# Kernel optimization log

Hardware: AMD Instinct MI355X
Metric: run time of the kernel (lower is better)

The kernel has to match this reference:

```python
import jax, jax.numpy as jnp
import numpy as np

B, SM, SI, D, H, FF = 4, 1024, 4096, 256, 8, 1024
EPS = 1e-6

def _ln(x, g, b):
    m = jnp.mean(x, axis=-1, keepdims=True)
    v = jnp.mean(jnp.square(x - m), axis=-1, keepdims=True)
    return (x - m) * jax.lax.rsqrt(v + EPS) * g + b

def setup_inputs() -> dict:
    key = jax.random.key(0)
    ks = jax.random.split(key, 12)
    s = 0.02
    return {
        "state_seq": jax.random.normal(ks[0], (B, SM, D), jnp.float32),
        "input_seq": jax.random.normal(ks[1], (B, SI, D), jnp.float32),
        "Wk": jax.random.normal(ks[2], (D, D), jnp.float32) * s,
        "bk": jnp.zeros((D,), jnp.float32),
        "Wv": jax.random.normal(ks[3], (D, D), jnp.float32) * s,
        "bv": jnp.zeros((D,), jnp.float32),
        "Wq": jax.random.normal(ks[4], (H, D, D), jnp.float32) * s,
        "bq": jnp.zeros((H, D), jnp.float32),
        "Wo": jax.random.normal(ks[5], (H * D, D), jnp.float32) * s,
        "bo": jnp.zeros((D,), jnp.float32),
        "ln1_g": jnp.ones((D,), jnp.float32),
        "ln1_b": jnp.zeros((D,), jnp.float32),
        "W_in": jax.random.normal(ks[6], (D, FF), jnp.float32) * s,
        "b_in": jnp.zeros((FF,), jnp.float32),
        "Wg_nl": jax.random.normal(ks[7], (FF, FF), jnp.float32) * s,
        "bg_nl": jnp.zeros((FF,), jnp.float32),
        "Wg_l": jax.random.normal(ks[8], (FF, FF), jnp.float32) * s,
        "bg_l": jnp.zeros((FF,), jnp.float32),
        "Wg_o": jax.random.normal(ks[9], (FF, D), jnp.float32) * s,
        "bg_o": jnp.zeros((D,), jnp.float32),
        "ln2_g": jnp.ones((D,), jnp.float32),
        "ln2_b": jnp.zeros((D,), jnp.float32),
    }

def reference(state_seq, input_seq, Wk, bk, Wv, bv, Wq, bq, Wo, bo,
              ln1_g, ln1_b, W_in, b_in, Wg_nl, bg_nl, Wg_l, bg_l, Wg_o, bg_o,
              ln2_g, ln2_b):
    # shared key/value projections (multi-query: one K/V, many Q)
    ik = input_seq @ Wk + bk            # [B,SI,D]
    mk = state_seq @ Wk + bk            # [B,SM,D]
    iv = input_seq @ Wv + bv            # [B,SI,D]
    mv = state_seq @ Wv + bv            # [B,SM,D]
    # per-head queries from memory cells, stacked over H
    q = jnp.einsum('bmd,hde->hbme', state_seq, Wq) + bq[:, None, None, :]  # [H,B,SM,D]
    input_score = jnp.einsum('hbme,bse->hbms', q, ik)                      # [H,B,SM,SI]
    self_score = jnp.sum(q * mk[None], axis=-1, keepdims=True)             # [H,B,SM,1]
    score = jnp.concatenate([self_score, input_score], axis=-1)
    score = score / jnp.sqrt(jnp.asarray(D, score.dtype))
    attn = jax.nn.softmax(score, axis=-1)                                  # [H,B,SM,1+SI]
    val = jnp.einsum('hbms,bse->hbme', attn[..., 1:], iv) + attn[..., 0:1] * mv[None]
    concat = jnp.transpose(val, (1, 2, 0, 3)).reshape(val.shape[1], val.shape[2], -1)  # [B,SM,H*D]
    attn_out = concat @ Wo + bo
    x = _ln(attn_out + state_seq, ln1_g, ln1_b)
    h = jax.nn.relu(x @ W_in + b_in)                                       # [B,SM,FF]
    g = jax.nn.relu(h @ Wg_nl + bg_nl) * (h @ Wg_l + bg_l)
    ff = g @ Wg_o + bg_o
    return _ln(ff + x, ln2_g, ln2_b)
```

## Files before the change

kernel.cpp:

```cpp
#include <hip/hip_runtime.h>
#include <hip/hip_bf16.h>

typedef __bf16 bfx8 __attribute__((ext_vector_type(8)));
typedef __bf16 bfx4 __attribute__((ext_vector_type(4)));
typedef float  f32x4 __attribute__((ext_vector_type(4)));
typedef float  f32x16 __attribute__((ext_vector_type(16)));

#define MFMA16(a,b,c) __builtin_amdgcn_mfma_f32_16x16x32_bf16((a),(b),(c),0,0,0)
#define MFMA32(a,b,c) __builtin_amdgcn_mfma_f32_32x32x16_bf16((a),(b),(c),0,0,0)


#define PSCALE 0.09016844f
#define PCLAMP 43.2808512f

__device__ __forceinline__ unsigned cvtpk_bf16(float lo, float hi) {
  unsigned d;
  asm("v_cvt_pk_bf16_f32 %0, %1, %2" : "=v"(d) : "v"(lo), "v"(hi));
  return d;
}

__device__ __forceinline__ bfx8 packswap(const float* p) {
  unsigned a = cvtpk_bf16(p[0], p[1]);
  unsigned b = cvtpk_bf16(p[2], p[3]);
  unsigned c = cvtpk_bf16(p[4], p[5]);
  unsigned d = cvtpk_bf16(p[6], p[7]);
  asm("v_permlane32_swap_b32 %0, %1" : "+v"(a), "+v"(c));
  asm("v_permlane32_swap_b32 %0, %1" : "+v"(b), "+v"(d));
  union { unsigned u[4]; bfx8 v; } uu;
  uu.u[0] = a; uu.u[1] = b; uu.u[2] = c; uu.u[3] = d;
  return uu.v;
}

__device__ __forceinline__ void tile_tr(const float* __restrict__ src, __bf16* __restrict__ dst,
                                        int R, int C, int tile, float (*lt)[65]) {
  int tpr = C >> 6;
  int tr = tile / tpr, tc = tile % tpr;
  int c  = threadIdx.x & 63;
  int r0 = (threadIdx.x >> 6) << 4;
  const float* sp = src + (long)(tr * 64 + r0) * C + tc * 64 + c;
#pragma unroll
  for (int i = 0; i < 16; i++) lt[r0 + i][c] = sp[(long)i * C];
  __syncthreads();
  __bf16* dp = dst + (long)(tc * 64 + r0) * R + tr * 64 + c;
#pragma unroll
  for (int i = 0; i < 16; i++) dp[(long)i * R] = (__bf16)lt[c][r0 + i];
}

__global__ void trans_attn_t(const float* __restrict__ Wk, const float* __restrict__ Wv,
                             const float* __restrict__ Wq, const float* __restrict__ Wo,
                             __bf16* __restrict__ wkvqt, __bf16* __restrict__ wot) {
  __shared__ float lt[64][65];
  int t = blockIdx.x;
  if (t < 16)       tile_tr(Wk, wkvqt, 256, 256, t, lt);
  else if (t < 32)  tile_tr(Wv, wkvqt + 65536, 256, 256, t - 16, lt);
  else if (t < 160) {
    int e = t - 32, m = e >> 4;
    tile_tr(Wq + (long)m * 65536, wkvqt + 131072 + (long)m * 65536, 256, 256, e & 15, lt);
  } else            tile_tr(Wo, wot, 2048, 256, t - 160, lt);
}

__device__ __forceinline__
void gemm_body(const __bf16* __restrict__ Xb, const float* __restrict__ Xf,
               const __bf16* __restrict__ Wt,
               const float* __restrict__ b1, const float* __restrict__ b2,
               const float* __restrict__ b3,
               __bf16* __restrict__ C, __bf16* __restrict__ C2, __bf16* __restrict__ C3,
               float* __restrict__ Cf,
               int M, int N, int Kfull, int kspan, int xmode, int mode, int act,
               int bx, int by, int bz, __bf16* xs, __bf16* wsm) {
  const int tid  = threadIdx.x;
  const int lane = tid & 63;
  const int w    = tid >> 6;
  const int l15  = lane & 15;
  const int quad = lane >> 4;
  const int wm   = (w >> 1) * 64;
  const int wn   = (w & 1) * 64;
  const int m0   = bx * 128;
  const int n0   = by * 128;
  const int k0   = (mode == 7) ? bz * kspan : 0;

  f32x4 acc[4][4];
#pragma unroll
  for (int i = 0; i < 4; i++)
#pragma unroll
    for (int j = 0; j < 4; j++) acc[i][j] = (f32x4){0.f, 0.f, 0.f, 0.f};

  for (int kk = k0; kk < k0 + kspan; kk += 64) {
    __syncthreads();
#pragma unroll
    for (int rep = 0; rep < 4; rep++) {
      int idx = rep * 256 + tid;
      int row = idx >> 3;
      int g   = idx & 7;
      if (xmode == 1) {
        const float* p = Xf + (long)(m0 + row) * Kfull + kk + g * 8;
        f32x4 a0 = *(const f32x4*)p;
        f32x4 a1 = *(const f32x4*)(p + 4);
        bfx8 v;
#pragma unroll
        for (int j = 0; j < 4; j++) { v[j] = (__bf16)a0[j]; v[4 + j] = (__bf16)a1[j]; }
        *(bfx8*)&xs[row * 72 + g * 8] = v;
      } else if (xmode == 2) {
        const __bf16* p = Xb + (long)(m0 + row) * 2048 + kk + g * 8;
        bfx8 a = *(const bfx8*)p;
        bfx8 bb = *(const bfx8*)(p + 1024);
        bfx8 v;
#pragma unroll
        for (int j = 0; j < 8; j++) v[j] = (__bf16)((float)a[j] * (float)bb[j]);
        *(bfx8*)&xs[row * 72 + g * 8] = v;
      } else {
        *(bfx8*)&xs[row * 72 + g * 8] = *(const bfx8*)(Xb + (long)(m0 + row) * Kfull + kk + g * 8);
      }
      *(bfx8*)&wsm[row * 72 + g * 8] = *(const bfx8*)(Wt + (long)(n0 + row) * Kfull + kk + g * 8);
    }
    __syncthreads();
#pragma unroll
    for (int ks = 0; ks < 2; ks++) {
      bfx8 af[4], bf_[4];
#pragma unroll
      for (int i = 0; i < 4; i++) af[i]  = *(const bfx8*)&xs[(wm + 16 * i + l15) * 72 + ks * 32 + quad * 8];
#pragma unroll
      for (int j = 0; j < 4; j++) bf_[j] = *(const bfx8*)&wsm[(wn + 16 * j + l15) * 72 + ks * 32 + quad * 8];
#pragma unroll
      for (int i = 0; i < 4; i++)
#pragma unroll
        for (int j = 0; j < 4; j++) acc[i][j] = MFMA16(af[i], bf_[j], acc[i][j]);
    }
  }

#pragma unroll
  for (int j = 0; j < 4; j++) {
    int n = n0 + wn + 16 * j + l15;
    float bv;
    if (mode == 4)      bv = (n < 256) ? b1[n] : b2[n - 256];
    else if (mode == 5) bv = (n < 256) ? b1[n] : (n < 512) ? b2[n - 256] : b3[n - 512];
    else if (mode == 6) bv = (n < 1024) ? b1[n] : b2[n - 1024];
    else if (mode == 7) bv = (bz == 0) ? b1[n] : 0.f;
    else                bv = b1[n];
#pragma unroll
    for (int i = 0; i < 4; i++) {
#pragma unroll
      for (int r = 0; r < 4; r++) {
        int m = m0 + wm + 16 * i + quad * 4 + r;
        float v = acc[i][j][r] + bv;
        if (mode == 6) { if (n < 1024) v = fmaxf(v, 0.f); }
        else if (act == 1) v = fmaxf(v, 0.f);
        if (mode == 4) {
          if (n < 256) C[(long)m * 256 + n] = (__bf16)v;
          else {
            int bb_ = m >> 12, si = m & 4095;
            C2[((long)(bb_ * 128 + (si >> 5)) * 256 + (n - 256)) * 32 + (si & 31)] = (__bf16)v;
          }
        } else if (mode == 5) {
          if (n < 256)      C[(long)m * 256 + n] = (__bf16)v;
          else if (n < 512) C2[(long)m * 256 + (n - 256)] = (__bf16)v;
          else {
            int nn = n - 512, hhh = nn >> 8, dd = nn & 255;
            C3[(long)hhh * 1048576 + (long)m * 256 + dd] = (__bf16)v;
          }
        } else if (mode == 7) {
          Cf[(long)bz * M * N + (long)m * N + n] = v;
        } else {
          C[(long)m * N + n] = (__bf16)v;
        }
      }
    }
  }
}

__global__ __launch_bounds__(256)
void gemm_bt(const __bf16* Xb, const float* Xf, const __bf16* Wt,
             const float* b1, const float* b2, const float* b3,
             __bf16* C, __bf16* C2, __bf16* C3, float* Cf,
             int M, int N, int Kfull, int kspan, int xmode, int mode, int act) {
  __shared__ __bf16 xs[128 * 72];
  __shared__ __bf16 wsm[128 * 72];
  gemm_body(Xb, Xf, Wt, b1, b2, b3, C, C2, C3, Cf, M, N, Kfull, kspan, xmode, mode, act,
            blockIdx.x, blockIdx.y, blockIdx.z, xs, wsm);
}

__global__ __launch_bounds__(256)
void proj2(const float* input, const float* state, const __bf16* Wkvqt,
           const float* bk, const float* bv, const float* bq,
           __bf16* ik, __bf16* ivT, __bf16* mk, __bf16* mv, __bf16* qbuf) {
  __shared__ __bf16 xs[128 * 72];
  __shared__ __bf16 wsm[128 * 72];
  int bid = blockIdx.x;
  if (bid < 512) {
    gemm_body(nullptr, input, Wkvqt, bk, bv, nullptr, ik, ivT, nullptr, nullptr,
              16384, 512, 256, 256, 1, 4, 0, bid & 127, bid >> 7, 0, xs, wsm);
  } else {
    int b2 = bid - 512;
    gemm_body(nullptr, state, Wkvqt, bk, bv, bq, mk, mv, qbuf, nullptr,
              4096, 2560, 256, 256, 1, 5, 0, b2 & 31, b2 >> 5, 0, xs, wsm);
  }
}

__global__ __launch_bounds__(256)
void attn_kernel(const __bf16* __restrict__ qb,
                 const __bf16* __restrict__ ik,
                 const __bf16* __restrict__ ivT,
                 const __bf16* __restrict__ mk,
                 const __bf16* __restrict__ mv,
                 __bf16* __restrict__ concat) {
  __shared__ __bf16 lk[2][32][264];
  __shared__ __bf16 lvt[3][256][40];

  const int tid  = threadIdx.x;
  const int lane = tid & 63;
  const int w    = tid >> 6;
  const int l31  = lane & 31;
  const int h    = lane >> 5;

  const int m0 = blockIdx.x * 128;
  const int b  = blockIdx.y;
  const int hh = blockIdx.z;
  const int mw = m0 + w * 32;

  const long qbase  = ((long)hh * 4096 + b * 1024 + mw) * 256;
  const long kvbase = (long)b * 4096 * 256;
  const long vtbase = (long)b * 128 * 8192;
  const long mbase  = ((long)b * 1024 + mw) * 256;

  bfx8 qf[16];
  {
    const __bf16* qrow = qb + qbase + (long)l31 * 256 + h * 8;
#pragma unroll
    for (int kt = 0; kt < 16; kt++) qf[kt] = *(const bfx8*)(qrow + kt * 16);
  }

  float ps_l;
  {
    const __bf16* krow = mk + mbase + (long)l31 * 256 + h * 8;
    float s = 0.f;
#pragma unroll
    for (int kt = 0; kt < 16; kt++) {
      bfx8 kv = *(const bfx8*)(krow + kt * 16);
#pragma unroll
      for (int j = 0; j < 8; j++) s += (float)qf[kt][j] * (float)kv[j];
    }
    s += __shfl_xor(s, 32);
    ps_l = __builtin_amdgcn_exp2f(fminf(s * PSCALE, PCLAMP));
  }

  f32x16 oacc[8];
#pragma unroll
  for (int dt = 0; dt < 8; dt++)
#pragma unroll
    for (int i = 0; i < 16; i++) oacc[dt][i] = 0.f;
  float den_l = 0.f;
  bfx8 pf0c, pf1c;

  f32x16 zz;
#pragma unroll
  for (int i = 0; i < 16; i++) zz[i] = 0.f;

  auto sload = [&](int c, bfx8* kreg, bfx8* vreg) {
    const long kb = kvbase + (long)c * 8192;
    const long vb = vtbase + (long)c * 8192;
#pragma unroll
    for (int rep = 0; rep < 4; rep++) {
      int idx = rep * 256 + tid;
      kreg[rep] = *(const bfx8*)(ik + kb + (long)(idx >> 5) * 256 + (idx & 31) * 8);
      vreg[rep] = *(const bfx8*)(ivT + vb + (long)idx * 8);
    }
  };
  auto sstore = [&](int kslot, int vslot, const bfx8* kreg, const bfx8* vreg) {
#pragma unroll
    for (int rep = 0; rep < 4; rep++) {
      int idx = rep * 256 + tid;
      *(bfx8*)&lk[kslot][idx >> 5][(idx & 31) * 8] = kreg[rep];
      *(bfx8*)&lvt[vslot][idx >> 2][(idx & 3) * 8] = vreg[rep];
    }
  };

  auto chunkMFMA = [&](int vslot, int kslot, bool doS, bool doPV, f32x16* sa) {
#pragma unroll
    for (int t = 0; t < 8; t++) {
      bfx8 vf0, vf1, kf0, kf1;
      if (doPV) {
        vf0 = *(const bfx8*)&lvt[vslot][t * 32 + l31][h * 8];
        vf1 = *(const bfx8*)&lvt[vslot][t * 32 + l31][16 + h * 8];
      }
      if (doS) {
        kf0 = *(const bfx8*)&lk[kslot][l31][(2 * t) * 16 + h * 8];
        kf1 = *(const bfx8*)&lk[kslot][l31][(2 * t + 1) * 16 + h * 8];
      }
      if (doPV) oacc[t] = MFMA32(pf0c, vf0, oacc[t]);
      if (doS) {
        if (t < 2) sa[2 * t] = MFMA32(kf0, qf[2 * t], zz);
        else       sa[(2 * t) & 3] = MFMA32(kf0, qf[2 * t], sa[(2 * t) & 3]);
      }
      if (doPV) oacc[t] = MFMA32(pf1c, vf1, oacc[t]);
      if (doS) {
        if (t < 2) sa[2 * t + 1] = MFMA32(kf1, qf[2 * t + 1], zz);
        else       sa[(2 * t + 1) & 3] = MFMA32(kf1, qf[2 * t + 1], sa[(2 * t + 1) & 3]);
      }
    }
  };

  auto finishP = [&](const f32x16* sa) {
    float p[16];
#pragma unroll
    for (int r = 0; r < 16; r++) {
      float s = (sa[0][r] + sa[1][r]) + (sa[2][r] + sa[3][r]);
      p[r] = __builtin_amdgcn_exp2f(fminf(s * PSCALE, PCLAMP));
      den_l += p[r];
    }
    pf0c = packswap(p);
    pf1c = packswap(p + 8);
  };

  {
    bfx8 kreg[4], vreg[4];
    sload(0, kreg, vreg);
    sstore(0, 0, kreg, vreg);
    sload(1, kreg, vreg);
    sstore(1, 1, kreg, vreg);
  }
  __syncthreads();

  f32x16 sa[4];
  chunkMFMA(0, 0, true, false, sa);
  finishP(sa);
  __syncthreads();

  int vcur = 0, vnst = 2;
  for (int i = 0; i < 126; i++) {
    bfx8 kreg[4], vreg[4];
    sload(i + 2, kreg, vreg);
    chunkMFMA(vcur, (i + 1) & 1, true, true, sa);
    sstore(i & 1, vnst, kreg, vreg);
    finishP(sa);
    __syncthreads();
    vcur = (vcur == 2) ? 0 : vcur + 1;
    vnst = (vnst == 2) ? 0 : vnst + 1;
  }
  chunkMFMA(0, 1, true, true, sa);
  finishP(sa);
  chunkMFMA(1, 0, false, true, sa);

  float tot = den_l + __shfl_xor(den_l, 32) + ps_l;
#pragma unroll
  for (int r = 0; r < 16; r++) {
    int row = (r & 3) + 8 * (r >> 2) + 4 * h;
    float ps   = __shfl(ps_l, row);
    float dinv = 1.f / __shfl(tot, row);
    const __bf16* mvrow = mv + mbase + (long)row * 256;
    __bf16* crow = concat + ((long)(b * 1024 + mw + row)) * 2048 + hh * 256;
#pragma unroll
    for (int dt = 0; dt < 8; dt++) {
      int d = dt * 32 + l31;
      crow[d] = (__bf16)((oacc[dt][r] + ps * (float)mvrow[d]) * dinv);
    }
  }
}

__device__ __forceinline__
void ln4_body(const float* __restrict__ parts, const float* __restrict__ res,
              const float* __restrict__ g, const float* __restrict__ beta,
              __bf16* __restrict__ outb, float* __restrict__ outf, int bid) {
  int row  = bid * 4 + (threadIdx.x >> 6);
  int lane = threadIdx.x & 63;
  const float* p = parts + (long)row * 256 + lane * 4;
  f32x4 a0 = *(const f32x4*)p;
  f32x4 a1 = *(const f32x4*)(p + 1048576);
  f32x4 a2 = *(const f32x4*)(p + 2097152);
  f32x4 a3 = *(const f32x4*)(p + 3145728);
  f32x4 rv = *(const f32x4*)(res + (long)row * 256 + lane * 4);
  float v[4], s1 = 0.f, s2 = 0.f;
#pragma unroll
  for (int i = 0; i < 4; i++) {
    v[i] = a0[i] + a1[i] + a2[i] + a3[i] + rv[i];
    s1 += v[i];
    s2 += v[i] * v[i];
  }
#pragma unroll
  for (int off = 32; off >= 1; off >>= 1) {
    s1 += __shfl_xor(s1, off);
    s2 += __shfl_xor(s2, off);
  }
  float mean = s1 * (1.f / 256.f);
  float var  = fmaxf(s2 * (1.f / 256.f) - mean * mean, 0.f);
  float rstd = rsqrtf(var + 1e-6f);
#pragma unroll
  for (int i = 0; i < 4; i++) {
    int c = lane * 4 + i;
    float o = (v[i] - mean) * rstd * g[c] + beta[c];
    if (outb) outb[(long)row * 256 + c] = (__bf16)o;
    if (outf) outf[(long)row * 256 + c] = o;
  }
}

__global__ __launch_bounds__(256)
void ln4_kernel(const float* __restrict__ parts, const float* __restrict__ res,
                const float* __restrict__ g, const float* __restrict__ beta,
                __bf16* __restrict__ outb, float* __restrict__ outf) {
  ln4_body(parts, res, g, beta, outb, outf, blockIdx.x);
}

__global__ __launch_bounds__(256)
void ln4_trffn(const float* __restrict__ parts, const float* __restrict__ res,
               const float* __restrict__ g, const float* __restrict__ beta,
               __bf16* __restrict__ outb, float* __restrict__ outf,
               const float* __restrict__ W_in, const float* __restrict__ Wg_nl,
               const float* __restrict__ Wg_l, const float* __restrict__ Wg_o,
               __bf16* __restrict__ wdst) {
  __shared__ float lt[64][65];
  int bid = blockIdx.x;
  if (bid < 1024) {
    ln4_body(parts, res, g, beta, outb, outf, bid);
  } else {
    int t = bid - 1024;
    if (t < 64)       tile_tr(W_in, wdst, 256, 1024, t, lt);
    else if (t < 320) tile_tr(Wg_nl, wdst + 262144, 1024, 1024, t - 64, lt);
    else if (t < 576) tile_tr(Wg_l, wdst + 1310720, 1024, 1024, t - 320, lt);
    else              tile_tr(Wg_o, wdst + 2359296, 1024, 256, t - 576, lt);
  }
}

extern "C" void kernel_launch(void* const* d_in, const int* in_sizes, int n_in,
                              void* d_out, int out_size, void* d_ws, size_t ws_size,
                              hipStream_t stream) {
  const float* state  = (const float*)d_in[0];
  const float* input  = (const float*)d_in[1];
  const float* Wk     = (const float*)d_in[2];
  const float* bk     = (const float*)d_in[3];
  const float* Wv     = (const float*)d_in[4];
  const float* bv     = (const float*)d_in[5];
  const float* Wq     = (const float*)d_in[6];
  const float* bq     = (const float*)d_in[7];
  const float* Wo     = (const float*)d_in[8];
  const float* bo     = (const float*)d_in[9];
  const float* ln1g   = (const float*)d_in[10];
  const float* ln1b   = (const float*)d_in[11];
  const float* W_in   = (const float*)d_in[12];
  const float* b_in   = (const float*)d_in[13];
  const float* Wg_nl  = (const float*)d_in[14];
  const float* bg_nl  = (const float*)d_in[15];
  const float* Wg_l   = (const float*)d_in[16];
  const float* bg_l   = (const float*)d_in[17];
  const float* Wg_o   = (const float*)d_in[18];
  const float* bg_o   = (const float*)d_in[19];
  const float* ln2g   = (const float*)d_in[20];
  const float* ln2b   = (const float*)d_in[21];
  float* out = (float*)d_out;

  const size_t needed_elems = 28442624;
  if (ws_size < needed_elems * sizeof(__bf16)) return;

  __bf16* ws = (__bf16*)d_ws;
  size_t off = 0;
  auto alloc = [&](size_t n) { __bf16* p = ws + off; off += n; return p; };
  __bf16* Wkvqt  = alloc(655360);
  __bf16* Wot    = alloc(524288);
  __bf16* ik     = alloc(4194304);
  __bf16* ivT    = alloc(4194304);
  __bf16* mk     = alloc(1048576);
  __bf16* mv     = alloc(1048576);
  __bf16* qbuf   = alloc(8388608);
  __bf16* concat = alloc(8388608);
  float*  wo_parts = (float*)qbuf;
  __bf16* x      = mv;
  __bf16* hbuf   = ik;
  __bf16* t12    = qbuf;
  float*  ff_parts = (float*)ik;
  __bf16* Wffn   = concat;
  float*  xf     = (float*)(concat + 3670016);

  dim3 blk(256);

  trans_attn_t<<<dim3(288), blk, 0, stream>>>(Wk, Wv, Wq, Wo, Wkvqt, Wot);

  proj2<<<dim3(1152), blk, 0, stream>>>(input, state, Wkvqt, bk, bv, bq,
                                        ik, ivT, mk, mv, qbuf);

  attn_kernel<<<dim3(8, 4, 8), blk, 0, stream>>>(qbuf, ik, ivT, mk, mv, concat);

  gemm_bt<<<dim3(32, 2, 4), blk, 0, stream>>>(concat, nullptr, Wot, bo, nullptr, nullptr,
                                              nullptr, nullptr, nullptr, wo_parts,
                                              4096, 256, 2048, 512, 0, 7, 0);
  ln4_trffn<<<dim3(1664), blk, 0, stream>>>(wo_parts, state, ln1g, ln1b, x, xf,
                                            W_in, Wg_nl, Wg_l, Wg_o, Wffn);

  gemm_bt<<<dim3(32, 8), blk, 0, stream>>>(x, nullptr, Wffn, b_in, nullptr, nullptr,
                                           hbuf, nullptr, nullptr, nullptr,
                                           4096, 1024, 256, 256, 0, 0, 1);
  gemm_bt<<<dim3(32, 16), blk, 0, stream>>>(hbuf, nullptr, Wffn + 262144, bg_nl, bg_l, nullptr,
                                            t12, nullptr, nullptr, nullptr,
                                            4096, 2048, 1024, 1024, 0, 6, 0);
  gemm_bt<<<dim3(32, 2, 4), blk, 0, stream>>>(t12, nullptr, Wffn + 2359296, bg_o, nullptr, nullptr,
                                              nullptr, nullptr, nullptr, ff_parts,
                                              4096, 256, 1024, 256, 2, 7, 0);
  ln4_kernel<<<dim3(1024), blk, 0, stream>>>(ff_parts, xf, ln2g, ln2b, nullptr, out);
}
```

Baseline: 450.8 us.

## Add 64-key-chunk attention kernel with double-buffered K/V pipeline

```diff
diff --git a/kernel.cpp b/kernel.cpp
--- a/kernel.cpp
+++ b/kernel.cpp
@@ -197,12 +197,212 @@
 }
 
 __global__ __launch_bounds__(256)
-void attn_kernel(const __bf16* __restrict__ qb,
-                 const __bf16* __restrict__ ik,
-                 const __bf16* __restrict__ ivT,
-                 const __bf16* __restrict__ mk,
-                 const __bf16* __restrict__ mv,
-                 __bf16* __restrict__ concat) {
+void attn_kernel64(const __bf16* __restrict__ qb,
+                   const __bf16* __restrict__ ik,
+                   const __bf16* __restrict__ ivT,
+                   const __bf16* __restrict__ mk,
+                   const __bf16* __restrict__ mv,
+                   __bf16* __restrict__ concat) {
+  __shared__ __bf16 lk[2][64][264];
+  __shared__ __bf16 lvt[2][256][72];
+
+  const int tid  = threadIdx.x;
+  const int lane = tid & 63;
+  const int w    = tid >> 6;
+  const int l31  = lane & 31;
+  const int h    = lane >> 5;
+
+  const int m0 = blockIdx.x * 128;
+  const int b  = blockIdx.y;
+  const int hh = blockIdx.z;
+  const int mw = m0 + w * 32;
+
+  const long qbase  = ((long)hh * 4096 + b * 1024 + mw) * 256;
+  const long kvbase = (long)b * 4096 * 256;
+  const long vtbase = (long)b * 128 * 8192;
+  const long mbase  = ((long)b * 1024 + mw) * 256;
+
+  bfx8 qf[16];
+  {
+    const __bf16* qrow = qb + qbase + (long)l31 * 256 + h * 8;
+#pragma unroll
+    for (int kt = 0; kt < 16; kt++) qf[kt] = *(const bfx8*)(qrow + kt * 16);
+  }
+
+  float ps_l;
+  {
+    const __bf16* krow = mk + mbase + (long)l31 * 256 + h * 8;
+    float s = 0.f;
+#pragma unroll
+    for (int kt = 0; kt < 16; kt++) {
+      bfx8 kv = *(const bfx8*)(krow + kt * 16);
+#pragma unroll
+      for (int j = 0; j < 8; j++) s += (float)qf[kt][j] * (float)kv[j];
+    }
+    s += __shfl_xor(s, 32);
+    ps_l = __builtin_amdgcn_exp2f(fminf(s * PSCALE, PCLAMP));
+  }
+
+  f32x16 oacc[8];
+#pragma unroll
+  for (int dt = 0; dt < 8; dt++)
+#pragma unroll
+    for (int i = 0; i < 16; i++) oacc[dt][i] = 0.f;
+  float den_l = 0.f;
+  bfx8 pfA[4], pfB[4];
+
+  f32x16 zz;
+#pragma unroll
+  for (int i = 0; i < 16; i++) zz[i] = 0.f;
+
+  auto sload_k32 = [&](int c32, bfx8* kreg) {
+    const long kb = kvbase + (long)c32 * 8192;
+#pragma unroll
+    for (int rep = 0; rep < 4; rep++) {
+      int idx = rep * 256 + tid;
+      kreg[rep] = *(const bfx8*)(ik + kb + (long)(idx >> 5) * 256 + (idx & 31) * 8);
+    }
+  };
+  auto sload_v32 = [&](int c32, bfx8* vreg) {
+    const long vb = vtbase + (long)c32 * 8192;
+#pragma unroll
+    for (int rep = 0; rep < 4; rep++) {
+      int idx = rep * 256 + tid;
+      vreg[rep] = *(const bfx8*)(ivT + vb + (long)idx * 8);
+    }
+  };
+  auto sstore_k32 = [&](int slot, int half, const bfx8* kreg) {
+#pragma unroll
+    for (int rep = 0; rep < 4; rep++) {
+      int idx = rep * 256 + tid;
+      *(bfx8*)&lk[slot][half * 32 + (idx >> 5)][(idx & 31) * 8] = kreg[rep];
+    }
+  };
+  auto sstore_v32 = [&](int slot, int half, const bfx8* vreg) {
+#pragma unroll
+    for (int rep = 0; rep < 4; rep++) {
+      int idx = rep * 256 + tid;
+      *(bfx8*)&lvt[slot][idx >> 2][half * 32 + (idx & 3) * 8] = vreg[rep];
+    }
+  };
+
+  auto phase = [&](int vslot, int kslot, int half, bool doS, bool doPV,
+                   const bfx8* pf, f32x16* sa) {
+#pragma unroll
+    for (int t = 0; t < 8; t++) {
+      bfx8 vf0, vf1, kf0, kf1;
+      if (doPV) {
+        vf0 = *(const bfx8*)&lvt[vslot][t * 32 + l31][half * 32 + h * 8];
+        vf1 = *(const bfx8*)&lvt[vslot][t * 32 + l31][half * 32 + 16 + h * 8];
+      }
+      if (doS) {
+        kf0 = *(const bfx8*)&lk[kslot][half * 32 + l31][(2 * t) * 16 + h * 8];
+        kf1 = *(const bfx8*)&lk[kslot][half * 32 + l31][(2 * t + 1) * 16 + h * 8];
+      }
+      if (doPV) oacc[t] = MFMA32(pf[0], vf0, oacc[t]);
+      if (doS) {
+        if (t < 2) sa[2 * t] = MFMA32(kf0, qf[2 * t], zz);
+        else       sa[(2 * t) & 3] = MFMA32(kf0, qf[2 * t], sa[(2 * t) & 3]);
+      }
+      if (doPV) oacc[t] = MFMA32(pf[1], vf1, oacc[t]);
+      if (doS) {
+        if (t < 2) sa[2 * t + 1] = MFMA32(kf1, qf[2 * t + 1], zz);
+        else       sa[(2 * t + 1) & 3] = MFMA32(kf1, qf[2 * t + 1], sa[(2 * t + 1) & 3]);
+      }
+    }
+  };
+
+  auto finishP = [&](const f32x16* sa, bfx8* pf) {
+    float p[16];
+#pragma unroll
+    for (int r = 0; r < 16; r++) {
+      float s = (sa[0][r] + sa[1][r]) + (sa[2][r] + sa[3][r]);
+      p[r] = __builtin_amdgcn_exp2f(fminf(s * PSCALE, PCLAMP));
+      den_l += p[r];
+    }
+    pf[0] = packswap(p);
+    pf[1] = packswap(p + 8);
+  };
+
+  f32x16 sa[4];
+
+  {
+    bfx8 kreg[8], vreg[8];
+    sload_k32(0, kreg);
+    sload_k32(1, kreg + 4);
+    sload_v32(0, vreg);
+    sload_v32(1, vreg + 4);
+    sstore_k32(0, 0, kreg);
+    sstore_k32(0, 1, kreg + 4);
+    sstore_v32(0, 0, vreg);
+    sstore_v32(0, 1, vreg + 4);
+    sload_k32(2, kreg);
+    sload_k32(3, kreg + 4);
+    sstore_k32(1, 0, kreg);
+    sstore_k32(1, 1, kreg + 4);
+  }
+  __syncthreads();
+  phase(0, 0, 0, true, false, nullptr, sa);
+  finishP(sa, pfA + 0);
+  phase(0, 0, 1, true, false, nullptr, sa);
+  finishP(sa, pfA + 2);
+  __syncthreads();
+
+  for (int i = 0; i < 62; i++) {
+    bfx8 kreg[8], vreg[8];
+    sload_k32(2 * (i + 2), kreg);
+    sload_k32(2 * (i + 2) + 1, kreg + 4);
+    sload_v32(2 * (i + 1), vreg);
+    sload_v32(2 * (i + 1) + 1, vreg + 4);
+    phase(i & 1, (i + 1) & 1, 0, true, true, pfA + 0, sa);
+    finishP(sa, pfB + 0);
+    phase(i & 1, (i + 1) & 1, 1, true, true, pfA + 2, sa);
+    finishP(sa, pfB + 2);
+    sstore_k32(i & 1, 0, kreg);
+    sstore_k32(i & 1, 1, kreg + 4);
+    sstore_v32((i + 1) & 1, 0, vreg);
+    sstore_v32((i + 1) & 1, 1, vreg + 4);
+    __syncthreads();
+#pragma unroll
+    for (int q = 0; q < 4; q++) pfA[q] = pfB[q];
+  }
+  {
+    bfx8 vreg[8];
+    sload_v32(126, vreg);
+    sload_v32(127, vreg + 4);
+    phase(0, 1, 0, true, true, pfA + 0, sa);
+    finishP(sa, pfB + 0);
+    phase(0, 1, 1, true, true, pfA + 2, sa);
+    finishP(sa, pfB + 2);
+    sstore_v32(1, 0, vreg);
+    sstore_v32(1, 1, vreg + 4);
+    __syncthreads();
+#pragma unroll
+    for (int q = 0; q < 4; q++) pfA[q] = pfB[q];
+  }
+  phase(1, 0, 0, false, true, pfA + 0, sa);
+  phase(1, 0, 1, false, true, pfA + 2, sa);
+
+  float tot = den_l + __shfl_xor(den_l, 32) + ps_l;
+#pragma unroll
+  for (int r = 0; r < 16; r++) {
+    int row = (r & 3) + 8 * (r >> 2) + 4 * h;
+    float ps   = __shfl(ps_l, row);
+    float dinv = 1.f / __shfl(tot, row);
+    const __bf16* mvrow = mv + mbase + (long)row * 256;
+    __bf16* crow = concat + ((long)(b * 1024 + mw + row)) * 2048 + hh * 256;
+#pragma unroll
+    for (int dt = 0; dt < 8; dt++) {
+      int d = dt * 32 + l31;
+      crow[d] = (__bf16)((oacc[dt][r] + ps * (float)mvrow[d]) * dinv);
+    }
+  }
+}
+
+__global__ __launch_bounds__(256)
+void attn_kernel(const __bf16* __restrict__ qb, const __bf16* __restrict__ ik,
+                 const __bf16* __restrict__ ivT, const __bf16* __restrict__ mk,
+                 const __bf16* __restrict__ mv, __bf16* __restrict__ concat) {
   __shared__ __bf16 lk[2][32][264];
   __shared__ __bf16 lvt[3][256][40];
 
@@ -468,6 +668,13 @@
   __bf16* Wffn   = concat;
   float*  xf     = (float*)(concat + 3670016);
 
+  static int use64 = -1;
+  if (use64 < 0) {
+    hipFuncAttributes fa{};
+    hipError_t e = hipFuncGetAttributes(&fa, (const void*)attn_kernel64);
+    use64 = (e == hipSuccess && fa.localSizeBytes <= 16) ? 1 : 0;
+  }
+
   dim3 blk(256);
 
   trans_attn_t<<<dim3(288), blk, 0, stream>>>(Wk, Wv, Wq, Wo, Wkvqt, Wot);
@@ -475,7 +682,10 @@
   proj2<<<dim3(1152), blk, 0, stream>>>(input, state, Wkvqt, bk, bv, bq,
                                         ik, ivT, mk, mv, qbuf);
 
-  attn_kernel<<<dim3(8, 4, 8), blk, 0, stream>>>(qbuf, ik, ivT, mk, mv, concat);
+  if (use64)
+    attn_kernel64<<<dim3(8, 4, 8), blk, 0, stream>>>(qbuf, ik, ivT, mk, mv, concat);
+  else
+    attn_kernel<<<dim3(8, 4, 8), blk, 0, stream>>>(qbuf, ik, ivT, mk, mv, concat);
 
   gemm_bt<<<dim3(32, 2, 4), blk, 0, stream>>>(concat, nullptr, Wot, bo, nullptr, nullptr,
                                               nullptr, nullptr, nullptr, wo_parts,
```

Measured after the change: 464.0 us. 2.9% more time.
